# Kernel tuning notes

Measured on AMD Instinct MI355X. Metric: run time of the kernel, lower is better.

Reference implementation:

```python
import jax, jax.numpy as jnp
import numpy as np

B = 64
RX, RZ, RX_, RZ_ = 32, 16, 16, 8
TN = 1
STRIDE = 2
IN_DIM, OUT_DIM = 256, 512
KEY_DIM, H, ATTN_RATIO = 32, 8, 2
D = ATTN_RATIO * KEY_DIM            # per-head value dim = 64
DH = D * H                          # 512
NH_KD = KEY_DIM * H                 # 256
N = RX * RX + TN * RZ * RZ          # 1280 tokens (search + template)
N_ = RX_ * RX_ + TN * RZ_ * RZ_     # 320 subsampled query tokens
SCALE = KEY_DIM ** -0.5
EPS = 1e-5


def linear_bn(x, W, gamma, beta):
    # Linear (no bias) followed by BatchNorm1d in training mode over (B*N, C)
    y = jnp.einsum('bnc,oc->bno', x, W)
    m = y.mean(axis=(0, 1))
    v = y.var(axis=(0, 1))  # biased variance, as torch BN uses for normalization
    return (y - m) * jax.lax.rsqrt(v + EPS) * gamma + beta


def subsample(x):
    # stride-subsample the search-region tokens and each template's tokens
    b, n, c = x.shape
    parts = [x[:, :RX * RX].reshape(b, RX, RX, c)[:, ::STRIDE, ::STRIDE].reshape(b, -1, c)]
    for i in range(TN):
        s = RX * RX + i * RZ * RZ
        z = x[:, s:s + RZ * RZ].reshape(b, RZ, RZ, c)[:, ::STRIDE, ::STRIDE].reshape(b, -1, c)
        parts.append(z)
    return jnp.concatenate(parts, axis=1)


def setup_inputs() -> dict:
    key = jax.random.key(0)
    ks = jax.random.split(key, 4)
    return {
        'x': jax.random.normal(ks[0], (B, N, IN_DIM), dtype=jnp.float32),
        'W_kv': jax.random.normal(ks[1], (NH_KD + DH, IN_DIM), dtype=jnp.float32) * 0.02,
        'g_kv': jnp.ones((NH_KD + DH,), jnp.float32),
        'b_kv': jnp.zeros((NH_KD + DH,), jnp.float32),
        'W_q': jax.random.normal(ks[2], (NH_KD, IN_DIM), dtype=jnp.float32) * 0.02,
        'g_q': jnp.ones((NH_KD,), jnp.float32),
        'b_q': jnp.zeros((NH_KD,), jnp.float32),
        'W_p': jax.random.normal(ks[3], (OUT_DIM, DH), dtype=jnp.float32) * 0.02,
        'g_p': jnp.ones((OUT_DIM,), jnp.float32),
        'b_p': jnp.zeros((OUT_DIM,), jnp.float32),
    }


def reference(x, W_kv, g_kv, b_kv, W_q, g_q, b_q, W_p, g_p, b_p):
    b = x.shape[0]
    # fused KV projection + BN, then split into per-head K and V
    kv = linear_bn(x, W_kv, g_kv, b_kv).reshape(b, N, H, KEY_DIM + D)
    k = kv[..., :KEY_DIM].transpose(0, 2, 1, 3)   # [B,H,N,key_dim]
    v = kv[..., KEY_DIM:].transpose(0, 2, 1, 3)   # [B,H,N,d]
    # Q: subsample tokens, then Linear_BN
    q = linear_bn(subsample(x), W_q, g_q, b_q).reshape(b, N_, H, KEY_DIM).transpose(0, 2, 1, 3)
    attn = jax.nn.softmax(jnp.einsum('bhqd,bhkd->bhqk', q, k) * SCALE, axis=-1)
    o = jnp.einsum('bhqk,bhkd->bhqd', attn, v).transpose(0, 2, 1, 3).reshape(b, N_, DH)
    return linear_bn(jax.nn.hard_swish(o), W_p, g_p, b_p)
```

## Files before the change

kernel.cpp:

```cpp
#include <hip/hip_runtime.h>
#include <hip/hip_bf16.h>
#include <math.h>

#define EPSF 1e-5f
#define SCALEF 0.17677669529663687f
#define LOG2E 1.4426950408889634f

typedef unsigned short u16;
typedef unsigned int u32;
typedef __attribute__((ext_vector_type(8))) short bf16x8;
typedef __attribute__((ext_vector_type(4))) float f32x4;

__device__ __forceinline__ float b2f(u16 u) {
    union { unsigned int i; float f; } v; v.i = ((unsigned int)u) << 16; return v.f;
}
__device__ __forceinline__ u16 f2b(float f) {
    union { float f; unsigned int i; } v; v.f = f;
    unsigned int x = v.i;
    return (u16)((x + 0x7fffu + ((x >> 16) & 1u)) >> 16);
}
__device__ __forceinline__ float fexp2(float x) {
#if __has_builtin(__builtin_amdgcn_exp2f)
    return __builtin_amdgcn_exp2f(x);
#else
    return exp2f(x);
#endif
}
__device__ __forceinline__ u32 cvtpk_bf16(float lo, float hi) {
    u32 r;
    asm("v_cvt_pk_bf16_f32 %0, %1, %2" : "=v"(r) : "v"(lo), "v"(hi));
    return r;
}
__device__ __forceinline__ void gload_lds16(const u16* __restrict__ g, u16* l) {
    __builtin_amdgcn_global_load_lds(
        (const __attribute__((address_space(1))) void*)g,
        (__attribute__((address_space(3))) void*)l, 16, 0, 0);
}

__global__ void convert_f32_bf16(const float* __restrict__ src, u16* __restrict__ dst, int n4) {
    int i = blockIdx.x * 256 + threadIdx.x;
    if (i >= n4) return;
    float4 v = ((const float4*)src)[i];
    ushort4 o;
    o.x = f2b(v.x); o.y = f2b(v.y); o.z = f2b(v.z); o.w = f2b(v.w);
    ((ushort4*)dst)[i] = o;
}

__global__ void convert_wkv_perm(const float* __restrict__ W, u16* __restrict__ out) {
    int r = blockIdx.x, cl = threadIdx.x;
    int src = (r < 256) ? ((r >> 5) * 96 + (r & 31))
                        : (((r - 256) >> 6) * 96 + 32 + ((r - 256) & 63));
    out[r * 256 + cl] = f2b(W[src * 256 + cl]);
}

__global__ void gather_sub_bf16(const u16* __restrict__ xb, u16* __restrict__ xsub, int n8) {
    int i = blockIdx.x * 256 + threadIdx.x;
    if (i >= n8) return;
    int e = i << 3;
    int row = e >> 8;
    int col = e & 255;
    int b = row / 320;
    int t = row - b * 320;
    int n;
    if (t < 256) n = ((t >> 4) << 6) + ((t & 15) << 1);
    else { int tt = t - 256; n = 1024 + ((tt >> 3) << 5) + ((tt & 7) << 1); }
    *(int4*)(xsub + e) = *(const int4*)(xb + ((size_t)(b * 1280 + n)) * 256 + col);
}

template<int MODE, int NT, int KC>
__global__ __launch_bounds__(256) void gemm_ls(const u16* __restrict__ A, const u16* __restrict__ Bw,
                                               void* __restrict__ Cv, void* __restrict__ C2v,
                                               int N, float* __restrict__ sums) {
    __shared__ u16 As[128 * 256];
    const int tid = threadIdx.x;
    const int wave = tid >> 6, lane = tid & 63;
    const int quad = lane >> 4, lc = lane & 15;
    const int wr = wave >> 1, wc = wave & 1;
    const int id = blockIdx.x;
    const int xcd = id & 7, l = id >> 3;
    const int mchunk = ((int)gridDim.x >> 3) / NT;
    const int m_t = xcd * mchunk + l / NT;
    const int n_t = l - (l / NT) * NT;
    const int m0 = m_t * 128, n0 = n_t * 128;

    const int r_in = lane >> 5;
    const int g_l  = lane & 31;
    const u16* Bp = Bw + (size_t)(n0 + wc * 64 + lc) * KC + quad * 8;

    f32x4 acc[4][4];
#pragma unroll
    for (int i = 0; i < 4; ++i)
#pragma unroll
        for (int j = 0; j < 4; ++j) acc[i][j] = (f32x4){0.f, 0.f, 0.f, 0.f};

    for (int kb = 0; kb < KC; kb += 256) {
        if (kb) __syncthreads();
#pragma unroll
        for (int s = 0; s < 16; ++s) {
            int Rb = wave * 32 + s * 2;
            int R  = Rb + r_in;
            int col = ((g_l ^ (R & 7)) << 3) + kb;
            gload_lds16(A + (size_t)(m0 + R) * KC + col, &As[Rb * 256]);
        }
        asm volatile("s_waitcnt vmcnt(0)" ::: "memory");
        __syncthreads();
#pragma unroll
        for (int t = 0; t < 8; ++t) {
            bf16x8 af[4], bfr[4];
#pragma unroll
            for (int mi = 0; mi < 4; ++mi) {
                int R = wr * 64 + mi * 16 + lc;
                int g = (t * 4 + quad) ^ (R & 7);
                af[mi] = *(const bf16x8*)&As[R * 256 + g * 8];
            }
#pragma unroll
            for (int ni = 0; ni < 4; ++ni)
                bfr[ni] = *(const bf16x8*)(Bp + (size_t)(ni * 16) * KC + kb + t * 32);
#pragma unroll
            for (int mi = 0; mi < 4; ++mi)
#pragma unroll
                for (int ni = 0; ni < 4; ++ni)
                    acc[mi][ni] = __builtin_amdgcn_mfma_f32_16x16x32_bf16(af[mi], bfr[ni], acc[mi][ni], 0, 0, 0);
        }
    }

    float ps[4], ps2[4];
#pragma unroll
    for (int ni = 0; ni < 4; ++ni) { ps[ni] = 0.f; ps2[ni] = 0.f; }
#pragma unroll
    for (int mi = 0; mi < 4; ++mi)
#pragma unroll
        for (int ni = 0; ni < 4; ++ni)
#pragma unroll
            for (int r = 0; r < 4; ++r) {
                float v = acc[mi][ni][r];
                ps[ni] += v; ps2[ni] += v * v;
            }
#pragma unroll
    for (int ni = 0; ni < 4; ++ni) {
        ps[ni]  += __shfl_xor(ps[ni], 16);  ps[ni]  += __shfl_xor(ps[ni], 32);
        ps2[ni] += __shfl_xor(ps2[ni], 16); ps2[ni] += __shfl_xor(ps2[ni], 32);
    }
    if (quad == 0) {
        int rep = m_t & 7;
#pragma unroll
        for (int ni = 0; ni < 4; ++ni) {
            int c = n0 + wc * 64 + ni * 16 + lc;
            atomicAdd(&sums[(rep * 2 + 0) * N + c], ps[ni]);
            atomicAdd(&sums[(rep * 2 + 1) * N + c], ps2[ni]);
        }
    }

    if (MODE == 0 || MODE == 1) {
#pragma unroll
        for (int mi = 0; mi < 4; ++mi)
#pragma unroll
            for (int ni = 0; ni < 4; ++ni)
#pragma unroll
                for (int r = 0; r < 4; ++r) {
                    int row = m0 + wr * 64 + mi * 16 + quad * 4 + r;
                    int cn  = n0 + wc * 64 + ni * 16 + lc;
                    float v = acc[mi][ni][r];
                    if (MODE == 1) ((float*)Cv)[(size_t)row * N + cn] = v;
                    else           ((u16*)Cv)[(size_t)row * N + cn] = f2b(v);
                }
    } else if (n0 < 256) {
        u16* Kr = (u16*)Cv;
#pragma unroll
        for (int mi = 0; mi < 4; ++mi)
#pragma unroll
            for (int r = 0; r < 4; ++r) {
                int t = m0 + wr * 64 + mi * 16 + quad * 4 + r;
                int kk = t & 31;
                int pr = (t & ~31) + ((kk & 4) << 2) + ((kk >> 3) << 2) + (kk & 3);
#pragma unroll
                for (int ni = 0; ni < 4; ++ni) {
                    int c = n0 + wc * 64 + ni * 16 + lc;
                    Kr[(size_t)pr * 256 + c] = f2b(acc[mi][ni][r]);
                }
            }
    } else {
        u16* Vt = (u16*)C2v;
#pragma unroll
        for (int mi = 0; mi < 4; ++mi)
#pragma unroll
            for (int ni = 0; ni < 4; ++ni) {
                int cp = n0 - 256 + wc * 64 + ni * 16 + lc;
                int t0 = m0 + wr * 64 + mi * 16 + quad * 4;
                uint2 w;
                w.x = cvtpk_bf16(acc[mi][ni][0], acc[mi][ni][1]);
                w.y = cvtpk_bf16(acc[mi][ni][2], acc[mi][ni][3]);
                *(uint2*)(Vt + (size_t)cp * 81920 + t0) = w;
            }
    }
}

__global__ void finalize_bn(const float* __restrict__ sum2, const float* __restrict__ g,
                            const float* __restrict__ beta, int cols, float inv_n, float scale,
                            float* __restrict__ AB, int kvperm) {
    int c = blockIdx.x * 256 + threadIdx.x;
    if (c >= cols) return;
    float s = 0.f, s2 = 0.f;
#pragma unroll
    for (int r = 0; r < 8; ++r) {
        s  += sum2[(r * 2 + 0) * cols + c];
        s2 += sum2[(r * 2 + 1) * cols + c];
    }
    int src = c;
    if (kvperm) {
        src = (c < 256) ? ((c >> 5) * 96 + (c & 31))
                        : (((c - 256) >> 6) * 96 + 32 + ((c - 256) & 63));
    }
    float m = s * inv_n;
    float var = s2 * inv_n - m * m;
    float a = g[src] * rsqrtf(var + EPSF) * scale;
    AB[c] = a;
    AB[cols + c] = beta[src] * scale - m * a;
}

__global__ __launch_bounds__(256, 2) void attn_kernel5(const u16* __restrict__ Kr, const u16* __restrict__ Vt,
                                                       const u16* __restrict__ q_raw,
                                                       const float* __restrict__ ABq,
                                                       const float* __restrict__ ABkv,
                                                       u16* __restrict__ o_act) {
    const int tid = threadIdx.x;
    const int wave = tid >> 6, lane = tid & 63;
    const int quad = lane >> 4, lc = lane & 15;
    const int h = blockIdx.x, b = blockIdx.y;

    float qa[8], qb[8];
#pragma unroll
    for (int j = 0; j < 8; ++j) {
        int c = h * 32 + quad * 8 + j;
        float ak = ABkv[c];
        qa[j] = ABq[c] * ak;
        qb[j] = ABq[256 + c] * ak;
    }
    bf16x8 qf[5];
#pragma unroll
    for (int j = 0; j < 5; ++j) {
        const u16* qs = q_raw + ((size_t)(b * 320 + j * 64 + wave * 16 + lc)) * 256 + h * 32 + quad * 8;
        union { int4 v; u16 u[8]; } ld; ld.v = *(const int4*)qs;
        union { bf16x8 v; u16 u[8]; } st;
#pragma unroll
        for (int jj = 0; jj < 8; ++jj) st.u[jj] = f2b(b2f(ld.u[jj]) * qa[jj] + qb[jj]);
        qf[j] = st.v;
    }

    const u16* Kp = Kr + (size_t)b * 1280 * 256 + (size_t)lc * 256 + h * 32 + quad * 8;
    const u16* Vp = Vt + ((size_t)(h * 64 + lc)) * 81920 + b * 1280 + quad * 8;

    f32x4 acc[5][4];
#pragma unroll
    for (int j = 0; j < 5; ++j)
#pragma unroll
        for (int i = 0; i < 4; ++i) acc[j][i] = (f32x4){0.f, 0.f, 0.f, 0.f};
    float lsum[5];
#pragma unroll
    for (int j = 0; j < 5; ++j) lsum[j] = 0.f;

    const f32x4 z = (f32x4){0.f, 0.f, 0.f, 0.f};
    for (int kc = 0; kc < 1280; kc += 32) {
        bf16x8 kfA = *(const bf16x8*)(Kp + (size_t)kc * 256);
        bf16x8 kfB = *(const bf16x8*)(Kp + (size_t)(kc + 16) * 256);
        bf16x8 vf0 = *(const bf16x8*)(Vp + kc);
        bf16x8 vf1 = *(const bf16x8*)(Vp + (size_t)16 * 81920 + kc);
        bf16x8 vf2 = *(const bf16x8*)(Vp + (size_t)32 * 81920 + kc);
        bf16x8 vf3 = *(const bf16x8*)(Vp + (size_t)48 * 81920 + kc);
        f32x4 s0[5], s1[5];
#pragma unroll
        for (int j = 0; j < 5; ++j) {
            s0[j] = __builtin_amdgcn_mfma_f32_16x16x32_bf16(kfA, qf[j], z, 0, 0, 0);
            s1[j] = __builtin_amdgcn_mfma_f32_16x16x32_bf16(kfB, qf[j], z, 0, 0, 0);
        }
#pragma unroll
        for (int j = 0; j < 5; ++j) {
            float p0 = fexp2(s0[j][0]);
            float p1 = fexp2(s0[j][1]);
            float p2 = fexp2(s0[j][2]);
            float p3 = fexp2(s0[j][3]);
            float p4 = fexp2(s1[j][0]);
            float p5 = fexp2(s1[j][1]);
            float p6 = fexp2(s1[j][2]);
            float p7 = fexp2(s1[j][3]);
            lsum[j] += ((p0 + p1) + (p2 + p3)) + ((p4 + p5) + (p6 + p7));
            union { u32 w[4]; bf16x8 v; } pf;
            pf.w[0] = cvtpk_bf16(p0, p1);
            pf.w[1] = cvtpk_bf16(p2, p3);
            pf.w[2] = cvtpk_bf16(p4, p5);
            pf.w[3] = cvtpk_bf16(p6, p7);
            acc[j][0] = __builtin_amdgcn_mfma_f32_16x16x32_bf16(vf0, pf.v, acc[j][0], 0, 0, 0);
            acc[j][1] = __builtin_amdgcn_mfma_f32_16x16x32_bf16(vf1, pf.v, acc[j][1], 0, 0, 0);
            acc[j][2] = __builtin_amdgcn_mfma_f32_16x16x32_bf16(vf2, pf.v, acc[j][2], 0, 0, 0);
            acc[j][3] = __builtin_amdgcn_mfma_f32_16x16x32_bf16(vf3, pf.v, acc[j][3], 0, 0, 0);
        }
    }
    float av[16], bv[16];
#pragma unroll
    for (int t = 0; t < 16; ++t) {
        int cv = 256 + h * 64 + (t >> 2) * 16 + quad * 4 + (t & 3);
        av[t] = ABkv[cv];
        bv[t] = ABkv[768 + cv];
    }
#pragma unroll
    for (int j = 0; j < 5; ++j) {
        float l = lsum[j];
        l += __shfl_xor(l, 16);
        l += __shfl_xor(l, 32);
        float inv = 1.f / l;
        int qrow = b * 320 + j * 64 + wave * 16 + lc;
        u16* dst = o_act + (size_t)qrow * 512 + h * 64 + quad * 4;
#pragma unroll
        for (int nt = 0; nt < 4; ++nt) {
            ushort4 st;
#pragma unroll
            for (int r = 0; r < 4; ++r) {
                float o = av[nt * 4 + r] * (acc[j][nt][r] * inv) + bv[nt * 4 + r];
                float hs = o * fminf(fmaxf(o + 3.f, 0.f), 6.f) * (1.f / 6.f);
                ((u16*)&st)[r] = f2b(hs);
            }
            *(ushort4*)(dst + nt * 16) = st;
        }
    }
}

__global__ void bn_apply_out(const float* __restrict__ praw, const float* __restrict__ ABp,
                             float* __restrict__ out, int n4) {
    int i = blockIdx.x * 256 + threadIdx.x;
    if (i >= n4) return;
    int e = i << 2;
    int c = e & 511;
    float4 v = ((const float4*)praw)[i];
    float4 o;
    o.x = v.x * ABp[c]     + ABp[512 + c];
    o.y = v.y * ABp[c + 1] + ABp[512 + c + 1];
    o.z = v.z * ABp[c + 2] + ABp[512 + c + 2];
    o.w = v.w * ABp[c + 3] + ABp[512 + c + 3];
    ((float4*)out)[i] = o;
}

extern "C" void kernel_launch(void* const* d_in, const int* in_sizes, int n_in,
                              void* d_out, int out_size, void* d_ws, size_t ws_size,
                              hipStream_t stream) {
    const float* x   = (const float*)d_in[0];
    const float* Wkv = (const float*)d_in[1];
    const float* gkv = (const float*)d_in[2];
    const float* bkv = (const float*)d_in[3];
    const float* Wq  = (const float*)d_in[4];
    const float* gq  = (const float*)d_in[5];
    const float* bq  = (const float*)d_in[6];
    const float* Wp  = (const float*)d_in[7];
    const float* gp  = (const float*)d_in[8];
    const float* bp  = (const float*)d_in[9];
    float* out = (float*)d_out;

    char* ws = (char*)d_ws;
    size_t off = 0;
    auto alloc = [&](size_t bytes) -> void* {
        void* p = ws + off;
        off += (bytes + 255) & ~(size_t)255;
        return p;
    };
    void*  slot1  = alloc(81920ull * 256 * 2);
    u16*   x_b    = (u16*)slot1;
    float* p_raw  = (float*)slot1;
    u16*   K_raw  = (u16*)alloc(81920ull * 256 * 2);
    u16*   Vt_raw = (u16*)alloc(512ull * 81920 * 2);
    u16*   q_raw  = (u16*)alloc(20480ull * 256 * 2);
    void*  slot2  = alloc(20480ull * 512 * 2);
    u16*   xsub_b = (u16*)slot2;
    u16*   o_act  = (u16*)slot2;
    u16*   Wkv_b  = (u16*)alloc(768ull * 256 * 2);
    u16*   Wq_b   = (u16*)alloc(256ull * 256 * 2);
    u16*   Wp_b   = (u16*)alloc(512ull * 512 * 2);
    float* sums_kv = (float*)alloc(8 * 2 * 768 * sizeof(float));
    float* sums_q  = (float*)alloc(8 * 2 * 256 * sizeof(float));
    float* sums_p  = (float*)alloc(8 * 2 * 512 * sizeof(float));
    float* ABkv = (float*)alloc(1536 * sizeof(float));
    float* ABq  = (float*)alloc(512 * sizeof(float));
    float* ABp  = (float*)alloc(1024 * sizeof(float));

    dim3 blk(256);
    hipMemsetAsync(sums_kv, 0, 8 * 2 * (768 + 256 + 512) * sizeof(float), stream);

    convert_f32_bf16<<<20480, blk, 0, stream>>>(x,   x_b,   5242880);
    convert_wkv_perm<<<768,   blk, 0, stream>>>(Wkv, Wkv_b);
    convert_f32_bf16<<<64,    blk, 0, stream>>>(Wq,  Wq_b,  16384);
    convert_f32_bf16<<<256,   blk, 0, stream>>>(Wp,  Wp_b,  65536);
    gather_sub_bf16<<<2560,   blk, 0, stream>>>(x_b, xsub_b, 655360);

    gemm_ls<2, 6, 256><<<3840, blk, 0, stream>>>(x_b,    Wkv_b, K_raw, Vt_raw, 768, sums_kv);
    gemm_ls<0, 2, 256><<<320,  blk, 0, stream>>>(xsub_b, Wq_b,  q_raw, nullptr, 256, sums_q);

    finalize_bn<<<3, blk, 0, stream>>>(sums_kv, gkv, bkv, 768, 1.f / 81920.f, 1.f, ABkv, 1);
    finalize_bn<<<1, blk, 0, stream>>>(sums_q,  gq,  bq,  256, 1.f / 20480.f, SCALEF * LOG2E, ABq, 0);

    attn_kernel5<<<dim3(8, 64), blk, 0, stream>>>(K_raw, Vt_raw, q_raw, ABq, ABkv, o_act);

    gemm_ls<1, 4, 512><<<640, blk, 0, stream>>>(o_act, Wp_b, p_raw, nullptr, 512, sums_p);
    finalize_bn<<<2, blk, 0, stream>>>(sums_p, gp, bp, 512, 1.f / 20480.f, 1.f, ABp, 0);

    bn_apply_out<<<10240, blk, 0, stream>>>(p_raw, ABp, out, 2621440);
}
```

Before: 380.4 us.

## Restructure projection GEMM into per-wave double-buffered LDS staging of A and B

Replaces the block-shared 128x256 A tile, loaded once per K chunk behind a block barrier, with per-wave private LDS buffers. Each wave stages its own 64x32 A and B slices with async global-to-LDS loads into two buffers, prefetching step t+1 while computing step t, and no __syncthreads is needed. B now goes through LDS instead of being read directly from global memory per fragment. The aim is to overlap memory latency with MFMA work and drop block barriers. In exchange, A rows are fetched redundantly by the two waves sharing a row band, B likewise, and the old XOR swizzle is gone, so LDS bank conflicts may rise.

Measured after the change: 349.5 us. -8.1%, faster.

```diff
diff --git a/kernel.cpp b/kernel.cpp
--- a/kernel.cpp
+++ b/kernel.cpp
@@ -68,10 +68,10 @@
 }
 
 template<int MODE, int NT, int KC>
-__global__ __launch_bounds__(256) void gemm_ls(const u16* __restrict__ A, const u16* __restrict__ Bw,
+__global__ __launch_bounds__(256) void gemm_wp(const u16* __restrict__ A, const u16* __restrict__ Bw,
                                                void* __restrict__ Cv, void* __restrict__ C2v,
                                                int N, float* __restrict__ sums) {
-    __shared__ u16 As[128 * 256];
+    __shared__ u16 L[4 * 8192];
     const int tid = threadIdx.x;
     const int wave = tid >> 6, lane = tid & 63;
     const int quad = lane >> 4, lc = lane & 15;
@@ -83,9 +83,11 @@
     const int n_t = l - (l / NT) * NT;
     const int m0 = m_t * 128, n0 = n_t * 128;
 
-    const int r_in = lane >> 5;
-    const int g_l  = lane & 31;
-    const u16* Bp = Bw + (size_t)(n0 + wc * 64 + lc) * KC + quad * 8;
+    u16* Lw = &L[wave * 8192];
+    const int srow = lane >> 2;
+    const int scol = (lane & 3) << 3;
+    const u16* gA = A  + (size_t)(m0 + wr * 64 + srow) * KC + scol;
+    const u16* gB = Bw + (size_t)(n0 + wc * 64 + srow) * KC + scol;
 
     f32x4 acc[4][4];
 #pragma unroll
@@ -93,35 +95,34 @@
 #pragma unroll
         for (int j = 0; j < 4; ++j) acc[i][j] = (f32x4){0.f, 0.f, 0.f, 0.f};
 
-    for (int kb = 0; kb < KC; kb += 256) {
-        if (kb) __syncthreads();
-#pragma unroll
-        for (int s = 0; s < 16; ++s) {
-            int Rb = wave * 32 + s * 2;
-            int R  = Rb + r_in;
-            int col = ((g_l ^ (R & 7)) << 3) + kb;
-            gload_lds16(A + (size_t)(m0 + R) * KC + col, &As[Rb * 256]);
-        }
-        asm volatile("s_waitcnt vmcnt(0)" ::: "memory");
-        __syncthreads();
-#pragma unroll
-        for (int t = 0; t < 8; ++t) {
-            bf16x8 af[4], bfr[4];
-#pragma unroll
-            for (int mi = 0; mi < 4; ++mi) {
-                int R = wr * 64 + mi * 16 + lc;
-                int g = (t * 4 + quad) ^ (R & 7);
-                af[mi] = *(const bf16x8*)&As[R * 256 + g * 8];
-            }
+    auto STAGE = [&](int buf, int t) {
+#pragma unroll
+        for (int s = 0; s < 4; ++s) {
+            gload_lds16(gA + (size_t)(s * 16) * KC + t * 32, Lw + buf * 4096 + s * 512);
+            gload_lds16(gB + (size_t)(s * 16) * KC + t * 32, Lw + buf * 4096 + 2048 + s * 512);
+        }
+    };
+
+    STAGE(0, 0);
+#pragma unroll
+    for (int t = 0; t < KC / 32; ++t) {
+        const int buf = t & 1;
+        if (t + 1 < KC / 32) {
+            STAGE(buf ^ 1, t + 1);
+            asm volatile("s_waitcnt vmcnt(8)" ::: "memory");
+        } else {
+            asm volatile("s_waitcnt vmcnt(0)" ::: "memory");
+        }
+        bf16x8 af[4], bfr[4];
+#pragma unroll
+        for (int mi = 0; mi < 4; ++mi) af[mi]  = *(const bf16x8*)&Lw[buf * 4096 + (mi * 16 + lc) * 32 + quad * 8];
+#pragma unroll
+        for (int ni = 0; ni < 4; ++ni) bfr[ni] = *(const bf16x8*)&Lw[buf * 4096 + 2048 + (ni * 16 + lc) * 32 + quad * 8];
+#pragma unroll
+        for (int mi = 0; mi < 4; ++mi)
 #pragma unroll
             for (int ni = 0; ni < 4; ++ni)
-                bfr[ni] = *(const bf16x8*)(Bp + (size_t)(ni * 16) * KC + kb + t * 32);
-#pragma unroll
-            for (int mi = 0; mi < 4; ++mi)
-#pragma unroll
-                for (int ni = 0; ni < 4; ++ni)
-                    acc[mi][ni] = __builtin_amdgcn_mfma_f32_16x16x32_bf16(af[mi], bfr[ni], acc[mi][ni], 0, 0, 0);
-        }
+                acc[mi][ni] = __builtin_amdgcn_mfma_f32_16x16x32_bf16(af[mi], bfr[ni], acc[mi][ni], 0, 0, 0);
     }
 
     float ps[4], ps2[4];
@@ -389,15 +390,15 @@
     convert_f32_bf16<<<256,   blk, 0, stream>>>(Wp,  Wp_b,  65536);
     gather_sub_bf16<<<2560,   blk, 0, stream>>>(x_b, xsub_b, 655360);
 
-    gemm_ls<2, 6, 256><<<3840, blk, 0, stream>>>(x_b,    Wkv_b, K_raw, Vt_raw, 768, sums_kv);
-    gemm_ls<0, 2, 256><<<320,  blk, 0, stream>>>(xsub_b, Wq_b,  q_raw, nullptr, 256, sums_q);
+    gemm_wp<2, 6, 256><<<3840, blk, 0, stream>>>(x_b,    Wkv_b, K_raw, Vt_raw, 768, sums_kv);
+    gemm_wp<0, 2, 256><<<320,  blk, 0, stream>>>(xsub_b, Wq_b,  q_raw, nullptr, 256, sums_q);
 
     finalize_bn<<<3, blk, 0, stream>>>(sums_kv, gkv, bkv, 768, 1.f / 81920.f, 1.f, ABkv, 1);
     finalize_bn<<<1, blk, 0, stream>>>(sums_q,  gq,  bq,  256, 1.f / 20480.f, SCALEF * LOG2E, ABq, 0);
 
     attn_kernel5<<<dim3(8, 64), blk, 0, stream>>>(K_raw, Vt_raw, q_raw, ABq, ABkv, o_act);
 
-    gemm_ls<1, 4, 512><<<640, blk, 0, stream>>>(o_act, Wp_b, p_raw, nullptr, 512, sums_p);
+    gemm_wp<1, 4, 512><<<640, blk, 0, stream>>>(o_act, Wp_b, p_raw, nullptr, 512, sums_p);
     finalize_bn<<<2, blk, 0, stream>>>(sums_p, gp, bp, 512, 1.f / 20480.f, 1.f, ABp, 0);
 
     bn_apply_out<<<10240, blk, 0, stream>>>(p_raw, ABp, out, 2621440);
```
